# Kernel tuning notes

Hardware: AMD Instinct MI355X
Metric: run time of the kernel (lower is better)

The kernel has to match this reference:

```python
import jax, jax.numpy as jnp
import numpy as np

B, T, C = 8, 2048, 768
N_LAYER, LAYER_ID = 12, 0


def setup_inputs() -> dict:
    key = jax.random.key(0)
    ks = jax.random.split(key, 5)
    s = 1.0 / np.sqrt(C)
    x = jax.random.normal(ks[0], (B, T, C), jnp.float32)
    Wk = jax.random.normal(ks[1], (C, C), jnp.float32) * s
    Wv = jax.random.normal(ks[2], (C, C), jnp.float32) * s
    Wr = jax.random.normal(ks[3], (C, C), jnp.float32) * s
    Wo = jax.random.normal(ks[4], (C, C), jnp.float32) * s
    # 'fancy' init for decay / first (layer_id=0 -> ratio_0_to_1 = 0)
    h = np.arange(C, dtype=np.float64)
    decay = (-5.0 + 8.0 * (h / (C - 1)) ** 0.7).astype(np.float32)
    zigzag = (((np.arange(C) + 1) % 3) - 1).astype(np.float64) * 0.5
    first = (np.log(0.3) + zigzag).astype(np.float32)
    return dict(x=x, Wk=Wk, Wv=Wv, Wr=Wr, Wo=Wo,
                decay=jnp.asarray(decay), first=jnp.asarray(first))


def _bi_wkv(w, u, k, v):
    """Bidirectional WKV (Vision-RWKV style), numerically stabilized scans.

    y_t = (sum_{i<t} e^{-(t-1-i)w + k_i} v_i + sum_{i>t} e^{-(i-1-t)w + k_i} v_i
           + e^{u + k_t} v_t) / (same with v_i -> 1).
    k, v: [B,T,C]; w, u: [C].
    """
    kT = jnp.swapaxes(k, 0, 1)  # [T,B,C]
    vT = jnp.swapaxes(v, 0, 1)
    Bb, Cc = kT.shape[1], kT.shape[2]
    NEG = jnp.float32(-1e38)

    def step(carry, inp):
        a, b, p = carry  # a = sum e^{x_i-p} v_i, b = sum e^{x_i-p}, p = running max
        kt, vt = inp
        out = (a, b, p)  # state covers strictly-earlier positions
        p_new = jnp.maximum(p - w, kt)
        e1 = jnp.exp(p - w - p_new)
        e2 = jnp.exp(kt - p_new)
        return (e1 * a + e2 * vt, e1 * b + e2, p_new), out

    init = (jnp.zeros((Bb, Cc), jnp.float32),
            jnp.zeros((Bb, Cc), jnp.float32),
            jnp.full((Bb, Cc), NEG, jnp.float32))
    _, (aL, bL, pL) = jax.lax.scan(step, init, (kT, vT))
    _, (aR, bR, pR) = jax.lax.scan(step, init, (kT[::-1], vT[::-1]))
    aR, bR, pR = aR[::-1], bR[::-1], pR[::-1]

    ps = u + kT  # self term exponent
    q = jnp.maximum(jnp.maximum(pL, pR), ps)
    eL = jnp.exp(pL - q)
    eR = jnp.exp(pR - q)
    eS = jnp.exp(ps - q)
    y = (eL * aL + eR * aR + eS * vT) / (eL * bL + eR * bR + eS)
    return jnp.swapaxes(y, 0, 1)  # [B,T,C]


def reference(x, Wk, Wv, Wr, Wo, decay, first):
    Tlen = x.shape[1]
    # shift_pixel=0 -> xk = xv = xr = x
    k = jnp.einsum('btc,oc->bto', x, Wk)
    v = jnp.einsum('btc,oc->bto', x, Wv)
    sr = jax.nn.sigmoid(jnp.einsum('btc,oc->bto', x, Wr))
    y = _bi_wkv(decay / Tlen, first / Tlen, k, v)
    return jnp.einsum('btj,cj->btc', sr * y, Wo)
```

## Files before the change

kernel.cpp:

```cpp
#include <hip/hip_runtime.h>

#define BSZ 8
#define TLEN 2048
#define CDIM 768
#define LCH 16
#define NCH (TLEN / LCH)

typedef __attribute__((ext_vector_type(4))) float f32x4;
typedef __attribute__((ext_vector_type(8))) _Float16 f16x8;
typedef __attribute__((ext_vector_type(4))) _Float16 f16x4;
typedef __attribute__((ext_vector_type(4))) float float4v;

#define GLD16(g, l)                                                          \
    __builtin_amdgcn_global_load_lds(                                        \
        (const __attribute__((address_space(1))) unsigned int*)(g),          \
        (__attribute__((address_space(3))) unsigned int*)(l), 16, 0, 0)

__global__ __launch_bounds__(256) void split_f16(const float* __restrict__ src,
                                                 _Float16* __restrict__ dst, int n4) {
    int i = blockIdx.x * 256 + threadIdx.x;
    if (i >= n4) return;
    float4v f = ((const float4v*)src)[i];
    f16x4 h;
    #pragma unroll
    for (int j = 0; j < 4; ++j) h[j] = (_Float16)f[j];
    ((f16x4*)dst)[i] = h;
}

__global__ __launch_bounds__(512, 2) void gemm_8ph(
    const _Float16* __restrict__ A, const _Float16* __restrict__ W,
    _Float16* __restrict__ o0, _Float16* __restrict__ o1, _Float16* __restrict__ o2,
    float* __restrict__ of32, int mpx, int NTL) {
    constexpr int K = CDIM;
    constexpr int NT = K / 64;
    __shared__ __align__(16) char smem[131072];

    const int tid  = threadIdx.x;
    const int lane = tid & 63;
    const int wid  = tid >> 6;
    const int bid  = blockIdx.x;
    const int xcd  = bid & 7;
    const int lj   = bid >> 3;
    const int mt   = lj / NTL;
    const int nt   = lj - mt * NTL;
    const int m0   = (xcd * mpx + mt) * 256;
    const int n0   = nt * 256;

    const int j0 = tid, j1 = tid + 512;
    const char* gA = (const char*)A;
    const char* gW = (const char*)W;
    const size_t gA0 = (size_t)(m0 + (j0 >> 2)) * (K * 2) + (j0 & 3) * 16;
    const size_t gA1 = (size_t)(m0 + (j1 >> 2)) * (K * 2) + (j1 & 3) * 16;
    const size_t gW0 = (size_t)(n0 + (j0 >> 2)) * (K * 2) + (j0 & 3) * 16;
    const size_t gW1 = (size_t)(n0 + (j1 >> 2)) * (K * 2) + (j1 & 3) * 16;

    auto STAGE_SEC = [&](int bufb, int p, int t) {
        const int ks = p >> 1;
        const int secb = bufb + (p & 1) * 16384 + ks * 32768;
        const size_t kb = (size_t)t * 128 + ks * 64;
        if ((p & 1) == 0) {
            GLD16(gA + gA0 + kb, &smem[secb] + j0 * 16);
            GLD16(gA + gA1 + kb, &smem[secb] + j1 * 16);
        } else {
            GLD16(gW + gW0 + kb, &smem[secb] + j0 * 16);
            GLD16(gW + gW1 + kb, &smem[secb] + j1 * 16);
        }
    };

    const int wr = wid >> 2;
    const int wc = wid & 3;
    const int rl = lane & 15;
    const int kc = (lane >> 4) << 4;

    f32x4 acc[8][4];
    #pragma unroll
    for (int i = 0; i < 8; ++i)
        #pragma unroll
        for (int j = 0; j < 4; ++j)
            acc[i][j] = (f32x4){0.f, 0.f, 0.f, 0.f};

    #pragma unroll
    for (int p = 0; p < 4; ++p) STAGE_SEC(0, p, 0);
    asm volatile("s_waitcnt vmcnt(0)" ::: "memory");
    __builtin_amdgcn_s_barrier();

    for (int t = 0; t < NT; ++t) {
        const int db  = (t & 1) << 16;
        const int nb2 = db ^ 65536;
        const char* sb = &smem[db];
        f16x8 breg[4];

        #pragma unroll
        for (int p = 0; p < 4; ++p) {
            const int ks = p >> 1, mh = p & 1;
            const char* asec = sb + ks * 32768;
            const char* bsec = sb + 16384 + ks * 32768;

            f16x8 areg[4];
            #pragma unroll
            for (int mi = 0; mi < 4; ++mi)
                areg[mi] = *(const f16x8*)(asec + (wr * 128 + (mh * 4 + mi) * 16 + rl) * 64 + kc);
            if (mh == 0) {
                #pragma unroll
                for (int nf = 0; nf < 4; ++nf)
                    breg[nf] = *(const f16x8*)(bsec + (wc * 64 + nf * 16 + rl) * 64 + kc);
            }
            if (t + 1 < NT) STAGE_SEC(nb2, p, t + 1);

            __builtin_amdgcn_s_barrier();
            asm volatile("s_waitcnt lgkmcnt(0)" ::: "memory");
            __builtin_amdgcn_sched_barrier(0);
            __builtin_amdgcn_s_setprio(1);
            #pragma unroll
            for (int mi = 0; mi < 4; ++mi)
                #pragma unroll
                for (int nf = 0; nf < 4; ++nf)
                    acc[mh * 4 + mi][nf] = __builtin_amdgcn_mfma_f32_16x16x32_f16(
                        areg[mi], breg[nf], acc[mh * 4 + mi][nf], 0, 0, 0);
            __builtin_amdgcn_s_setprio(0);
            if (t + 1 < NT) asm volatile("s_waitcnt vmcnt(4)" ::: "memory");
            else            asm volatile("s_waitcnt vmcnt(0)" ::: "memory");
            __builtin_amdgcn_s_barrier();
        }
    }

    const int erow0 = m0 + wr * 128 + ((lane >> 4) << 2);
    if (of32) {
        const int col0 = n0 + wc * 64 + rl;
        #pragma unroll
        for (int mf = 0; mf < 8; ++mf)
            #pragma unroll
            for (int nf = 0; nf < 4; ++nf)
                #pragma unroll
                for (int r = 0; r < 4; ++r)
                    of32[(size_t)(erow0 + mf * 16 + r) * CDIM + (col0 + nf * 16)] =
                        acc[mf][nf][r];
    } else {
        const int mat  = nt / 3;
        const int col0 = (nt - mat * 3) * 256 + wc * 64 + rl;
        _Float16* o = (mat == 0) ? o0 : ((mat == 1) ? o1 : o2);
        if (mat == 2) {
            #pragma unroll
            for (int mf = 0; mf < 8; ++mf)
                #pragma unroll
                for (int nf = 0; nf < 4; ++nf)
                    #pragma unroll
                    for (int r = 0; r < 4; ++r)
                        o[(size_t)(erow0 + mf * 16 + r) * CDIM + (col0 + nf * 16)] =
                            (_Float16)(1.0f / (1.0f + __expf(-acc[mf][nf][r])));
        } else {
            #pragma unroll
            for (int mf = 0; mf < 8; ++mf)
                #pragma unroll
                for (int nf = 0; nf < 4; ++nf)
                    #pragma unroll
                    for (int r = 0; r < 4; ++r)
                        o[(size_t)(erow0 + mf * 16 + r) * CDIM + (col0 + nf * 16)] =
                            (_Float16)acc[mf][nf][r];
        }
    }
}

#define WKV_STEP(a, bb, p, kt, vt, w)                \
    {                                                \
        const float pn = fmaxf((p) - (w), (kt));     \
        const float e1 = __expf((p) - (w) - pn);     \
        const float e2 = __expf((kt) - pn);          \
        (a)  = e1 * (a)  + e2 * (vt);                \
        (bb) = e1 * (bb) + e2;                       \
        (p)  = pn;                                   \
    }

__global__ __launch_bounds__(256) void wkv_phase1(
    const _Float16* __restrict__ k, const _Float16* __restrict__ v,
    const float* __restrict__ decay,
    float* __restrict__ Sfa, float* __restrict__ Sfb, float* __restrict__ Sfp,
    float* __restrict__ Sba, float* __restrict__ Sbb, float* __restrict__ Sbp) {
    const int c = blockIdx.x * 256 + threadIdx.x;
    const int j = blockIdx.y;
    const int b = blockIdx.z;
    const float w = decay[c] * (1.0f / (float)TLEN);

    const size_t base = ((size_t)b * TLEN + (size_t)j * LCH) * CDIM + c;
    float kt[LCH], vt[LCH];
    #pragma unroll
    for (int i = 0; i < LCH; ++i) {
        kt[i] = (float)k[base + (size_t)i * CDIM];
        vt[i] = (float)v[base + (size_t)i * CDIM];
    }

    const size_t idx = ((size_t)b * NCH + j) * CDIM + c;

    float a = 0.0f, bb = 0.0f, p = -1e38f;
    #pragma unroll
    for (int i = 0; i < LCH; ++i) WKV_STEP(a, bb, p, kt[i], vt[i], w);
    Sfa[idx] = a; Sfb[idx] = bb; Sfp[idx] = p;

    a = 0.0f; bb = 0.0f; p = -1e38f;
    #pragma unroll
    for (int i = LCH - 1; i >= 0; --i) WKV_STEP(a, bb, p, kt[i], vt[i], w);
    Sba[idx] = a; Sbb[idx] = bb; Sbp[idx] = p;
}

#define WKV_COMBINE(a, bb, p, as, bs, ps, wL)        \
    {                                                \
        const float pn = fmaxf((p) - (wL), (ps));    \
        const float e1 = __expf((p) - (wL) - pn);    \
        const float e2 = __expf((ps) - pn);          \
        (a)  = e1 * (a)  + e2 * (as);                \
        (bb) = e1 * (bb) + e2 * (bs);                \
        (p)  = pn;                                   \
    }

__global__ __launch_bounds__(64) void wkv_phase2(
    const float* __restrict__ Sfa, const float* __restrict__ Sfb, const float* __restrict__ Sfp,
    const float* __restrict__ Sba, const float* __restrict__ Sbb, const float* __restrict__ Sbp,
    const float* __restrict__ decay,
    float* __restrict__ Lina, float* __restrict__ Linb, float* __restrict__ Linp,
    float* __restrict__ Rina, float* __restrict__ Rinb, float* __restrict__ Rinp) {
    const int c = blockIdx.x * 64 + threadIdx.x;
    const int b = blockIdx.y;
    const int dir = blockIdx.z;
    const float wL = decay[c] * ((float)LCH / (float)TLEN);

    const float* Sa = dir ? Sba : Sfa;
    const float* Sb = dir ? Sbb : Sfb;
    const float* Sp = dir ? Sbp : Sfp;
    float* Oa = dir ? Rina : Lina;
    float* Ob = dir ? Rinb : Linb;
    float* Op = dir ? Rinp : Linp;

    const size_t base = (size_t)b * NCH * CDIM + c;
    auto IDX = [&](int j) {
        return base + (size_t)(dir ? (NCH - 1 - j) : j) * CDIM;
    };

    float gaA[4], gbA[4], gpA[4], gaB[4], gbB[4], gpB[4];
    #pragma unroll
    for (int u = 0; u < 4; ++u) {
        const size_t id = IDX(u);
        gaA[u] = Sa[id]; gbA[u] = Sb[id]; gpA[u] = Sp[id];
    }
    float a = 0.0f, bb = 0.0f, p = -1e38f;

    for (int jg = 0; jg < NCH; jg += 8) {
        #pragma unroll
        for (int u = 0; u < 4; ++u) {
            const size_t id = IDX(jg + 4 + u);
            gaB[u] = Sa[id]; gbB[u] = Sb[id]; gpB[u] = Sp[id];
        }
        #pragma unroll
        for (int u = 0; u < 4; ++u) {
            const size_t id = IDX(jg + u);
            Oa[id] = a; Ob[id] = bb; Op[id] = p;
            WKV_COMBINE(a, bb, p, gaA[u], gbA[u], gpA[u], wL);
        }
        if (jg + 8 < NCH) {
            #pragma unroll
            for (int u = 0; u < 4; ++u) {
                const size_t id = IDX(jg + 8 + u);
                gaA[u] = Sa[id]; gbA[u] = Sb[id]; gpA[u] = Sp[id];
            }
        }
        #pragma unroll
        for (int u = 0; u < 4; ++u) {
            const size_t id = IDX(jg + 4 + u);
            Oa[id] = a; Ob[id] = bb; Op[id] = p;
            WKV_COMBINE(a, bb, p, gaB[u], gbB[u], gpB[u], wL);
        }
    }
}

__global__ __launch_bounds__(256) void wkv_phase3(
    const _Float16* __restrict__ k, const _Float16* __restrict__ v,
    const _Float16* __restrict__ sr,
    const float* __restrict__ Lina, const float* __restrict__ Linb, const float* __restrict__ Linp,
    const float* __restrict__ Rina, const float* __restrict__ Rinb, const float* __restrict__ Rinp,
    const float* __restrict__ decay, const float* __restrict__ first,
    _Float16* __restrict__ zh) {
    const int c = blockIdx.x * 256 + threadIdx.x;
    const int j = blockIdx.y;
    const int b = blockIdx.z;
    const float w = decay[c] * (1.0f / (float)TLEN);
    const float u = first[c] * (1.0f / (float)TLEN);

    const size_t base = ((size_t)b * TLEN + (size_t)j * LCH) * CDIM + c;
    float kt[LCH], vt[LCH];
    #pragma unroll
    for (int i = 0; i < LCH; ++i) {
        kt[i] = (float)k[base + (size_t)i * CDIM];
        vt[i] = (float)v[base + (size_t)i * CDIM];
    }

    const size_t idx = ((size_t)b * NCH + j) * CDIM + c;

    float ar[LCH], br[LCH], pr[LCH];
    {
        float a = Rina[idx], bb = Rinb[idx], p = Rinp[idx];
        #pragma unroll
        for (int i = LCH - 1; i >= 0; --i) {
            ar[i] = a; br[i] = bb; pr[i] = p;
            WKV_STEP(a, bb, p, kt[i], vt[i], w);
        }
    }
    {
        float a = Lina[idx], bb = Linb[idx], p = Linp[idx];
        #pragma unroll
        for (int i = 0; i < LCH; ++i) {
            const size_t off = base + (size_t)i * CDIM;
            const float srt = (float)sr[off];
            const float ps = u + kt[i];
            const float q  = fmaxf(fmaxf(p, pr[i]), ps);
            const float eL = __expf(p - q);
            const float eR = __expf(pr[i] - q);
            const float eS = __expf(ps - q);
            const float num = eL * a  + eR * ar[i] + eS * vt[i];
            const float den = eL * bb + eR * br[i] + eS;
            zh[off] = (_Float16)(srt * (num / den));
            WKV_STEP(a, bb, p, kt[i], vt[i], w);
        }
    }
}

extern "C" void kernel_launch(void* const* d_in, const int* in_sizes, int n_in,
                              void* d_out, int out_size, void* d_ws, size_t ws_size,
                              hipStream_t stream) {
    const float* x     = (const float*)d_in[0];
    const float* Wk    = (const float*)d_in[1];
    const float* Wv    = (const float*)d_in[2];
    const float* Wr    = (const float*)d_in[3];
    const float* Wo    = (const float*)d_in[4];
    const float* decay = (const float*)d_in[5];
    const float* first = (const float*)d_in[6];
    float* out = (float*)d_out;

    const size_t WN = (size_t)CDIM * CDIM;
    const size_t wbytes = 4 * WN * sizeof(_Float16);
    const size_t per_b  = (size_t)TLEN * CDIM * 8 + 12ull * NCH * CDIM * 4;
    if (ws_size < wbytes + per_b) return;
    int nb = (int)((ws_size - wbytes) / per_b);
    if (nb > BSZ) nb = BSZ;

    _Float16* wsp  = (_Float16*)d_ws;
    _Float16* Wcat = wsp;
    _Float16* Woh  = wsp + 3 * WN;

    const size_t NE = (size_t)nb * TLEN * CDIM;
    const size_t NP = (size_t)nb * NCH * CDIM;
    float* Sfa = (float*)(wsp + 4 * WN);
    float* Sfb = Sfa + NP;  float* Sfp = Sfb + NP;
    float* Sba = Sfp + NP;  float* Sbb = Sba + NP;  float* Sbp = Sbb + NP;
    float* Lina = Sbp + NP; float* Linb = Lina + NP; float* Linp = Linb + NP;
    float* Rina = Linp + NP; float* Rinb = Rina + NP; float* Rinp = Rinb + NP;
    _Float16* kh  = (_Float16*)(Rinp + NP);
    _Float16* vh  = kh + NE;
    _Float16* srh = vh + NE;
    _Float16* xh  = srh + NE;
    _Float16* zh  = xh;

    split_f16<<<dim3((int)(WN / 1024)), dim3(256), 0, stream>>>(Wk, Wcat + 0 * WN, (int)(WN / 4));
    split_f16<<<dim3((int)(WN / 1024)), dim3(256), 0, stream>>>(Wv, Wcat + 1 * WN, (int)(WN / 4));
    split_f16<<<dim3((int)(WN / 1024)), dim3(256), 0, stream>>>(Wr, Wcat + 2 * WN, (int)(WN / 4));
    split_f16<<<dim3((int)(WN / 1024)), dim3(256), 0, stream>>>(Wo, Woh, (int)(WN / 4));

    for (int b0 = 0; b0 < BSZ; b0 += nb) {
        const int curb = (BSZ - b0 < nb) ? (BSZ - b0) : nb;
        const int rows = curb * TLEN;
        const float* xc = x   + (size_t)b0 * TLEN * CDIM;
        float*       oc = out + (size_t)b0 * TLEN * CDIM;

        const int n4 = rows * CDIM / 4;
        split_f16<<<dim3(n4 / 256), dim3(256), 0, stream>>>(xc, xh, n4);

        const int mtiles = rows / 256;
        const int mpx    = mtiles / 8;

        gemm_8ph<<<dim3(mtiles * 9), dim3(512), 0, stream>>>(
            xh, Wcat, kh, vh, srh, nullptr, mpx, 9);

        wkv_phase1<<<dim3(CDIM / 256, NCH, curb), dim3(256), 0, stream>>>(
            kh, vh, decay, Sfa, Sfb, Sfp, Sba, Sbb, Sbp);
        wkv_phase2<<<dim3(CDIM / 64, curb, 2), dim3(64), 0, stream>>>(
            Sfa, Sfb, Sfp, Sba, Sbb, Sbp, decay,
            Lina, Linb, Linp, Rina, Rinb, Rinp);
        wkv_phase3<<<dim3(CDIM / 256, NCH, curb), dim3(256), 0, stream>>>(
            kh, vh, srh, Lina, Linb, Linp, Rina, Rinb, Rinp, decay, first, zh);

        gemm_8ph<<<dim3(mtiles * 3), dim3(512), 0, stream>>>(
            zh, Woh, nullptr, nullptr, nullptr, oc, mpx, 3);
    }
}
```

Measured before the change: 191.3 us.

## Replace 256x256 GEMM with 128x128 tiled kernel using XOR-swizzled LDS

Replaces the 512-thread 256x256-tile GEMM with a 256-thread 128x128-tile kernel. It stages A and W into an XOR-swizzled LDS layout to avoid bank conflicts, and uses a simpler double-buffered loop with __syncthreads instead of the hand-scheduled phase pipeline with setprio. The smaller tiles give four times as many blocks, which should improve load balance and occupancy across the CUs. The cost is less operand reuse per tile and the loss of the fine-grained load/compute interleaving.

```diff
diff --git a/kernel.cpp b/kernel.cpp
--- a/kernel.cpp
+++ b/kernel.cpp
@@ -27,13 +27,13 @@
     ((f16x4*)dst)[i] = h;
 }
 
-__global__ __launch_bounds__(512, 2) void gemm_8ph(
+__global__ __launch_bounds__(256, 2) void gemm_128(
     const _Float16* __restrict__ A, const _Float16* __restrict__ W,
     _Float16* __restrict__ o0, _Float16* __restrict__ o1, _Float16* __restrict__ o2,
     float* __restrict__ of32, int mpx, int NTL) {
     constexpr int K = CDIM;
     constexpr int NT = K / 64;
-    __shared__ __align__(16) char smem[131072];
+    __shared__ __align__(16) char smem[65536];
 
     const int tid  = threadIdx.x;
     const int lane = tid & 63;
@@ -43,92 +43,74 @@
     const int lj   = bid >> 3;
     const int mt   = lj / NTL;
     const int nt   = lj - mt * NTL;
-    const int m0   = (xcd * mpx + mt) * 256;
-    const int n0   = nt * 256;
-
-    const int j0 = tid, j1 = tid + 512;
+    const int m0   = (xcd * mpx + mt) * 128;
+    const int n0   = nt * 128;
+
+    const int gq = (tid & 7) ^ ((tid >> 3) & 7);
     const char* gA = (const char*)A;
     const char* gW = (const char*)W;
-    const size_t gA0 = (size_t)(m0 + (j0 >> 2)) * (K * 2) + (j0 & 3) * 16;
-    const size_t gA1 = (size_t)(m0 + (j1 >> 2)) * (K * 2) + (j1 & 3) * 16;
-    const size_t gW0 = (size_t)(n0 + (j0 >> 2)) * (K * 2) + (j0 & 3) * 16;
-    const size_t gW1 = (size_t)(n0 + (j1 >> 2)) * (K * 2) + (j1 & 3) * 16;
-
-    auto STAGE_SEC = [&](int bufb, int p, int t) {
-        const int ks = p >> 1;
-        const int secb = bufb + (p & 1) * 16384 + ks * 32768;
-        const size_t kb = (size_t)t * 128 + ks * 64;
-        if ((p & 1) == 0) {
-            GLD16(gA + gA0 + kb, &smem[secb] + j0 * 16);
-            GLD16(gA + gA1 + kb, &smem[secb] + j1 * 16);
-        } else {
-            GLD16(gW + gW0 + kb, &smem[secb] + j0 * 16);
-            GLD16(gW + gW1 + kb, &smem[secb] + j1 * 16);
+    const size_t gofsA = (size_t)(m0 + (tid >> 3)) * (K * 2) + gq * 16;
+    const size_t gofsB = (size_t)(n0 + (tid >> 3)) * (K * 2) + gq * 16;
+    const int lofs = tid * 16;
+
+    auto STAGE = [&](int bufb, int t) {
+        const size_t kb = (size_t)t * 128;
+        #pragma unroll
+        for (int q = 0; q < 4; ++q) {
+            GLD16(gA + gofsA + kb + (size_t)q * 49152, &smem[bufb] + lofs + q * 4096);
+            GLD16(gW + gofsB + kb + (size_t)q * 49152, &smem[bufb + 16384] + lofs + q * 4096);
         }
     };
 
-    const int wr = wid >> 2;
-    const int wc = wid & 3;
+    const int wr = wid >> 1, wc = wid & 1;
     const int rl = lane & 15;
-    const int kc = (lane >> 4) << 4;
-
-    f32x4 acc[8][4];
-    #pragma unroll
-    for (int i = 0; i < 8; ++i)
+    const int kc0 = ((((lane >> 4)    ) ^ (rl & 7)) << 4);
+    const int kc1 = ((((lane >> 4) + 4) ^ (rl & 7)) << 4);
+
+    f32x4 acc[4][4];
+    #pragma unroll
+    for (int i = 0; i < 4; ++i)
         #pragma unroll
         for (int j = 0; j < 4; ++j)
             acc[i][j] = (f32x4){0.f, 0.f, 0.f, 0.f};
 
-    #pragma unroll
-    for (int p = 0; p < 4; ++p) STAGE_SEC(0, p, 0);
-    asm volatile("s_waitcnt vmcnt(0)" ::: "memory");
-    __builtin_amdgcn_s_barrier();
-
+    auto COMPUTE = [&](int bufb) {
+        const char* sa = &smem[bufb];
+        const char* sbb = &smem[bufb + 16384];
+        #pragma unroll
+        for (int ks = 0; ks < 2; ++ks) {
+            const int kc = ks ? kc1 : kc0;
+            f16x8 a[4], b[4];
+            #pragma unroll
+            for (int fi = 0; fi < 4; ++fi)
+                a[fi] = *(const f16x8*)(sa + (wr * 64 + fi * 16 + rl) * 128 + kc);
+            #pragma unroll
+            for (int fj = 0; fj < 4; ++fj)
+                b[fj] = *(const f16x8*)(sbb + (wc * 64 + fj * 16 + rl) * 128 + kc);
+            #pragma unroll
+            for (int fi = 0; fi < 4; ++fi)
+                #pragma unroll
+                for (int fj = 0; fj < 4; ++fj)
+                    acc[fi][fj] = __builtin_amdgcn_mfma_f32_16x16x32_f16(
+                        a[fi], b[fj], acc[fi][fj], 0, 0, 0);
+        }
+    };
+
+    STAGE(0, 0);
+    __syncthreads();
+    int buf = 0;
     for (int t = 0; t < NT; ++t) {
-        const int db  = (t & 1) << 16;
-        const int nb2 = db ^ 65536;
-        const char* sb = &smem[db];
-        f16x8 breg[4];
-
-        #pragma unroll
-        for (int p = 0; p < 4; ++p) {
-            const int ks = p >> 1, mh = p & 1;
-            const char* asec = sb + ks * 32768;
-            const char* bsec = sb + 16384 + ks * 32768;
-
-            f16x8 areg[4];
-            #pragma unroll
-            for (int mi = 0; mi < 4; ++mi)
-                areg[mi] = *(const f16x8*)(asec + (wr * 128 + (mh * 4 + mi) * 16 + rl) * 64 + kc);
-            if (mh == 0) {
-                #pragma unroll
-                for (int nf = 0; nf < 4; ++nf)
-                    breg[nf] = *(const f16x8*)(bsec + (wc * 64 + nf * 16 + rl) * 64 + kc);
-            }
-            if (t + 1 < NT) STAGE_SEC(nb2, p, t + 1);
-
-            __builtin_amdgcn_s_barrier();
-            asm volatile("s_waitcnt lgkmcnt(0)" ::: "memory");
-            __builtin_amdgcn_sched_barrier(0);
-            __builtin_amdgcn_s_setprio(1);
-            #pragma unroll
-            for (int mi = 0; mi < 4; ++mi)
-                #pragma unroll
-                for (int nf = 0; nf < 4; ++nf)
-                    acc[mh * 4 + mi][nf] = __builtin_amdgcn_mfma_f32_16x16x32_f16(
-                        areg[mi], breg[nf], acc[mh * 4 + mi][nf], 0, 0, 0);
-            __builtin_amdgcn_s_setprio(0);
-            if (t + 1 < NT) asm volatile("s_waitcnt vmcnt(4)" ::: "memory");
-            else            asm volatile("s_waitcnt vmcnt(0)" ::: "memory");
-            __builtin_amdgcn_s_barrier();
-        }
-    }
-
-    const int erow0 = m0 + wr * 128 + ((lane >> 4) << 2);
+        if (t + 1 < NT) STAGE(buf ^ 32768, t + 1);
+        COMPUTE(buf);
+        __syncthreads();
+        buf ^= 32768;
+    }
+
+    const int erow0 = m0 + wr * 64 + ((lane >> 4) << 2);
     if (of32) {
         const int col0 = n0 + wc * 64 + rl;
         #pragma unroll
-        for (int mf = 0; mf < 8; ++mf)
+        for (int mf = 0; mf < 4; ++mf)
             #pragma unroll
             for (int nf = 0; nf < 4; ++nf)
                 #pragma unroll
@@ -136,12 +118,12 @@
                     of32[(size_t)(erow0 + mf * 16 + r) * CDIM + (col0 + nf * 16)] =
                         acc[mf][nf][r];
     } else {
-        const int mat  = nt / 3;
-        const int col0 = (nt - mat * 3) * 256 + wc * 64 + rl;
+        const int mat  = nt / 6;
+        const int col0 = (nt - mat * 6) * 128 + wc * 64 + rl;
         _Float16* o = (mat == 0) ? o0 : ((mat == 1) ? o1 : o2);
         if (mat == 2) {
             #pragma unroll
-            for (int mf = 0; mf < 8; ++mf)
+            for (int mf = 0; mf < 4; ++mf)
                 #pragma unroll
                 for (int nf = 0; nf < 4; ++nf)
                     #pragma unroll
@@ -150,7 +132,7 @@
                             (_Float16)(1.0f / (1.0f + __expf(-acc[mf][nf][r])));
         } else {
             #pragma unroll
-            for (int mf = 0; mf < 8; ++mf)
+            for (int mf = 0; mf < 4; ++mf)
                 #pragma unroll
                 for (int nf = 0; nf < 4; ++nf)
                     #pragma unroll
@@ -372,11 +354,11 @@
         const int n4 = rows * CDIM / 4;
         split_f16<<<dim3(n4 / 256), dim3(256), 0, stream>>>(xc, xh, n4);
 
-        const int mtiles = rows / 256;
+        const int mtiles = rows / 128;
         const int mpx    = mtiles / 8;
 
-        gemm_8ph<<<dim3(mtiles * 9), dim3(512), 0, stream>>>(
-            xh, Wcat, kh, vh, srh, nullptr, mpx, 9);
+        gemm_128<<<dim3(mtiles * 18), dim3(256), 0, stream>>>(
+            xh, Wcat, kh, vh, srh, nullptr, mpx, 18);
 
         wkv_phase1<<<dim3(CDIM / 256, NCH, curb), dim3(256), 0, stream>>>(
             kh, vh, decay, Sfa, Sfb, Sfp, Sba, Sbb, Sbp);
@@ -386,7 +368,7 @@
         wkv_phase3<<<dim3(CDIM / 256, NCH, curb), dim3(256), 0, stream>>>(
             kh, vh, srh, Lina, Linb, Linp, Rina, Rinb, Rinp, decay, first, zh);
 
-        gemm_8ph<<<dim3(mtiles * 3), dim3(512), 0, stream>>>(
-            zh, Woh, nullptr, nullptr, nullptr, oc, mpx, 3);
-    }
-}
+        gemm_128<<<dim3(mtiles * 6), dim3(256), 0, stream>>>(
+            zh, Woh, nullptr, nullptr, nullptr, oc, mpx, 6);
+    }
+}
```

Result: faster. 169.6 us (-11.4%).
